# Kernel tuning notes

Hardware: AMD Instinct MI355X
Metric: run time of the kernel (lower is better)

Reference implementation:

```python
import jax, jax.numpy as jnp
import numpy as np

H = 64  # hidden size
T, B, I = 512, 4096, 2


def gru_layer(x_seq, Wih, Whh, bih, bhh):
    """PyTorch-semantics GRU layer. x_seq: [T,B,in]. Returns (all_h [T,B,H], h_last [B,H])."""
    # Precompute input-side gates for all timesteps in one GEMM: [T,B,3H]
    xg = jnp.einsum('tbi,gi->tbg', x_seq, Wih) + bih
    h0 = jnp.zeros((x_seq.shape[1], H), dtype=x_seq.dtype)

    def step(h, xg_t):
        hg = h @ Whh.T + bhh  # [B,3H]
        r = jax.nn.sigmoid(xg_t[:, :H] + hg[:, :H])
        z = jax.nn.sigmoid(xg_t[:, H:2 * H] + hg[:, H:2 * H])
        n = jnp.tanh(xg_t[:, 2 * H:] + r * hg[:, 2 * H:])
        h_new = (1.0 - z) * n + z * h
        return h_new, h_new

    h_last, hs = jax.lax.scan(step, h0, xg)
    return hs, h_last


def setup_inputs() -> dict:
    key = jax.random.key(0)
    ks = jax.random.split(key, 12)
    s = 0.125  # ~1/sqrt(H), matches PyTorch uniform init scale
    inp = {
        'x': jax.random.normal(ks[0], (T, B, I), dtype=jnp.float32),
        'Wih0': jax.random.normal(ks[1], (3 * H, I), dtype=jnp.float32) * s,
        'Whh0': jax.random.normal(ks[2], (3 * H, H), dtype=jnp.float32) * s,
        'bih0': jax.random.normal(ks[3], (3 * H,), dtype=jnp.float32) * s,
        'bhh0': jax.random.normal(ks[4], (3 * H,), dtype=jnp.float32) * s,
        'Wih1': jax.random.normal(ks[5], (3 * H, H), dtype=jnp.float32) * s,
        'Whh1': jax.random.normal(ks[6], (3 * H, H), dtype=jnp.float32) * s,
        'bih1': jax.random.normal(ks[7], (3 * H,), dtype=jnp.float32) * s,
        'bhh1': jax.random.normal(ks[8], (3 * H,), dtype=jnp.float32) * s,
        'Wp': jax.random.normal(ks[9], (1, 2 * H), dtype=jnp.float32) * s,
        'bp': jax.random.normal(ks[10], (1,), dtype=jnp.float32) * s,
    }
    return inp


def reference(x, Wih0, Whh0, bih0, bhh0, Wih1, Whh1, bih1, bhh1, Wp, bp):
    hs0, h0f = gru_layer(x, Wih0, Whh0, bih0, bhh0)     # layer 0 over input
    _, h1f = gru_layer(hs0, Wih1, Whh1, bih1, bhh1)      # layer 1 over layer-0 outputs
    feat = jnp.concatenate([h0f, h1f], axis=-1)          # h_n.permute(1,0,2).flatten(1) -> [B, 2H]
    out = feat @ Wp.T + bp                               # [B,1]
    return out.reshape(-1)
```

## Files before the change

### kernel.cpp

```cpp
#include <hip/hip_runtime.h>
#include <stdint.h>

#define TSTEPS 512
#define BATCH  4096
#define SROW 76

typedef __attribute__((ext_vector_type(8))) short bf16x8;
typedef __attribute__((ext_vector_type(4))) float f32x4;
typedef __attribute__((ext_vector_type(2))) float f32x2;

#define SRZ (-1.4426950408889634f)
#define SN  ( 2.8853900817779268f)

struct PX { f32x2 gr0, gz0, gn0, gr1, gz1, gn1; };

__device__ __forceinline__ short f2bf(float f) {
    uint32_t u = __float_as_uint(f);
    uint32_t r = (u + 0x7fffu + ((u >> 16) & 1u)) >> 16;
    return (short)r;
}
__device__ __forceinline__ uint32_t cvt_pk_bf16(float a, float b) {
    uint32_t r;
    asm("v_cvt_pk_bf16_f32 %0, %1, %2" : "=v"(r) : "v"(a), "v"(b));
    return r;
}
__device__ __forceinline__ float fast_rcp(float x) { return __builtin_amdgcn_rcpf(x); }
#if __has_builtin(__builtin_amdgcn_exp2f)
__device__ __forceinline__ float exp2_fast(float x) { return __builtin_amdgcn_exp2f(x); }
#else
__device__ __forceinline__ float exp2_fast(float x) { return __expf(x * 0.6931471805599453f); }
#endif

__device__ __forceinline__ f32x2 fma2(f32x2 a, f32x2 b, f32x2 c) {
    return __builtin_elementwise_fma(a, b, c);
}
__device__ __forceinline__ f32x2 splat2(float s) { return (f32x2){s, s}; }
__device__ __forceinline__ f32x2 exp22(f32x2 y) {
    return (f32x2){exp2_fast(y[0]), exp2_fast(y[1])};
}
__device__ __forceinline__ f32x2 rcp2(f32x2 y) {
    return (f32x2){fast_rcp(y[0]), fast_rcp(y[1])};
}
__device__ __forceinline__ f32x2 sig2(f32x2 y) {
    return rcp2(exp22(y) + splat2(1.0f));
}
__device__ __forceinline__ f32x2 gru_h(f32x2 yz, f32x2 yn, f32x2 h) {
    const f32x2 A = exp22(yz);
    const f32x2 B = exp22(yn);
    const f32x2 P = A * B;
    const f32x2 u = (P - A) + fma2(h, B, h);
    const f32x2 d = (P + A) + (B + splat2(1.0f));
    return u * rcp2(d);
}
__device__ __forceinline__ void bar_lgkm() {
    asm volatile("s_waitcnt lgkmcnt(0)\n\ts_barrier" ::: "memory");
}

__global__ __launch_bounds__(512, 2) void gru_fused(
    const float* __restrict__ x,
    const float* __restrict__ Wih0,
    const float* __restrict__ Whh0,
    const float* __restrict__ bih0,
    const float* __restrict__ bhh0,
    const float* __restrict__ Wih1,
    const float* __restrict__ Whh1,
    const float* __restrict__ bih1,
    const float* __restrict__ bhh1,
    const float* __restrict__ Wp,
    const float* __restrict__ bp,
    float* __restrict__ out)
{
    const int tid  = threadIdx.x;
    const int wv   = tid >> 6;
    const int isL0 = (wv < 4);
    const int w4   = wv & 3;
    const int l    = tid & 63;
    const int lm   = l & 15;
    const int lq   = l >> 4;
    const int b0   = blockIdx.x * 16;
    const int j    = w4 * 16 + lm;

    __shared__ short h0A[2][16 * SROW];
    __shared__ short h1A[2][16 * SROW];
    __shared__ float Pf[16][64];

    for (int idx = tid; idx < 2 * 16 * SROW; idx += 512) {
        ((short*)h0A)[idx] = 0;
        ((short*)h1A)[idx] = 0;
    }
    __syncthreads();

    const int aoff = lm * SROW + lq * 8;
    const int r0   = lq * 4;

    if (isL0) {
        bf16x8 w0[3][2];
#pragma unroll
        for (int g = 0; g < 3; ++g) {
            const int row = g * 64 + j;
            const float sc = (g == 2) ? SN : SRZ;
#pragma unroll
            for (int q = 0; q < 2; ++q) {
                const float* p = Whh0 + row * 64 + q * 32 + lq * 8;
                bf16x8 vh;
#pragma unroll
                for (int i = 0; i < 8; ++i) vh[i] = f2bf(p[i] * sc);
                w0[g][q] = vh;
            }
        }
        const f32x2 wr0 = splat2(SRZ * Wih0[j * 2 + 0]), wr1 = splat2(SRZ * Wih0[j * 2 + 1]);
        const f32x2 wz0 = splat2(SRZ * Wih0[(64 + j) * 2 + 0]), wz1 = splat2(SRZ * Wih0[(64 + j) * 2 + 1]);
        const f32x2 wn0 = splat2(SN * Wih0[(128 + j) * 2 + 0]), wn1 = splat2(SN * Wih0[(128 + j) * 2 + 1]);
        const float cb[3] = { SRZ * (bih0[j] + bhh0[j]),
                              SRZ * (bih0[64 + j] + bhh0[64 + j]),
                              SN  * bhh0[128 + j] };
        const f32x2 bn = splat2(SN * bih0[128 + j]);

        f32x2 h01 = {0.f, 0.f}, h23 = {0.f, 0.f};

        const float* xb_ = x + (size_t)(b0 + r0) * 2;
        f32x4 xEa = *(const f32x4*)xb_;
        f32x4 xEb = *(const f32x4*)(xb_ + 4);
        f32x4 xOa = *(const f32x4*)(xb_ + (size_t)BATCH * 2);
        f32x4 xOb = *(const f32x4*)(xb_ + (size_t)BATCH * 2 + 4);
        const float* xp = xb_ + 2 * (size_t)BATCH * 2;

        PX pE, pO;
        {
            const f32x2 x0a = {xEa[0], xEa[2]}, x1a = {xEa[1], xEa[3]};
            const f32x2 x0b = {xEb[0], xEb[2]}, x1b = {xEb[1], xEb[3]};
            pE.gr0 = fma2(wr0, x0a, wr1 * x1a);
            pE.gz0 = fma2(wz0, x0a, wz1 * x1a);
            pE.gn0 = fma2(wn0, x0a, fma2(wn1, x1a, bn));
            pE.gr1 = fma2(wr0, x0b, wr1 * x1b);
            pE.gz1 = fma2(wz0, x0b, wz1 * x1b);
            pE.gn1 = fma2(wn0, x0b, fma2(wn1, x1b, bn));
        }

        auto l0_step = [&](int pr, bool doload, PX& u, PX& d,
                           f32x4& xla, f32x4& xlb,
                           const f32x4& xsa, const f32x4& xsb) {
            const int pw = pr ^ 1;
            const bf16x8 a00 = *(const bf16x8*)&h0A[pr][aoff];
            const bf16x8 a01 = *(const bf16x8*)&h0A[pr][aoff + 32];
            if (doload) {
                xla = *(const f32x4*)xp;
                xlb = *(const f32x4*)(xp + 4);
                xp += (size_t)BATCH * 2;
            }
            f32x4 hg0[3];
            __builtin_amdgcn_s_setprio(1);
#pragma unroll
            for (int g = 0; g < 3; ++g) {
                const f32x4 ci = {cb[g], cb[g], cb[g], cb[g]};
                f32x4 c;
                c = __builtin_amdgcn_mfma_f32_16x16x32_bf16(a00, w0[g][0], ci, 0, 0, 0);
                hg0[g] = __builtin_amdgcn_mfma_f32_16x16x32_bf16(a01, w0[g][1], c, 0, 0, 0);
            }
            __builtin_amdgcn_s_setprio(0);
            {
                const f32x2 x0a = {xsa[0], xsa[2]}, x1a = {xsa[1], xsa[3]};
                const f32x2 x0b = {xsb[0], xsb[2]}, x1b = {xsb[1], xsb[3]};
                d.gr0 = fma2(wr0, x0a, wr1 * x1a);
                d.gz0 = fma2(wz0, x0a, wz1 * x1a);
                d.gn0 = fma2(wn0, x0a, fma2(wn1, x1a, bn));
                d.gr1 = fma2(wr0, x0b, wr1 * x1b);
                d.gz1 = fma2(wz0, x0b, wz1 * x1b);
                d.gn1 = fma2(wn0, x0b, fma2(wn1, x1b, bn));
            }
            {
                const f32x2 hgr = {hg0[0][0], hg0[0][1]};
                const f32x2 hgz = {hg0[1][0], hg0[1][1]};
                const f32x2 hgn = {hg0[2][0], hg0[2][1]};
                const f32x2 rv = sig2(hgr + u.gr0);
                const f32x2 hv = gru_h(hgz + u.gz0, fma2(rv, hgn, u.gn0), h01);
                h01 = hv;
                const uint32_t pk = cvt_pk_bf16(hv[0], hv[1]);
                h0A[pw][(r0 + 0) * SROW + j] = (short)(pk & 0xffffu);
                h0A[pw][(r0 + 1) * SROW + j] = (short)(pk >> 16);
            }
            {
                const f32x2 hgr = {hg0[0][2], hg0[0][3]};
                const f32x2 hgz = {hg0[1][2], hg0[1][3]};
                const f32x2 hgn = {hg0[2][2], hg0[2][3]};
                const f32x2 rv = sig2(hgr + u.gr1);
                const f32x2 hv = gru_h(hgz + u.gz1, fma2(rv, hgn, u.gn1), h23);
                h23 = hv;
                const uint32_t pk = cvt_pk_bf16(hv[0], hv[1]);
                h0A[pw][(r0 + 2) * SROW + j] = (short)(pk & 0xffffu);
                h0A[pw][(r0 + 3) * SROW + j] = (short)(pk >> 16);
            }
        };

        for (int tp = 0; tp < TSTEPS / 2; ++tp) {
            const bool doload = (tp < TSTEPS / 2 - 1);
            l0_step(0, doload, pE, pO, xEa, xEb, xOa, xOb);
            bar_lgkm();
            l0_step(1, doload, pO, pE, xOa, xOb, xEa, xEb);
            bar_lgkm();
        }

        const float wp0 = Wp[j];
        Pf[r0 + 0][j] = wp0 * h01[0];
        Pf[r0 + 1][j] = wp0 * h01[1];
        Pf[r0 + 2][j] = wp0 * h23[0];
        Pf[r0 + 3][j] = wp0 * h23[1];
        __syncthreads();
        __syncthreads();
    } else {
        bf16x8 w1[3][2], w2[3][2];
#pragma unroll
        for (int g = 0; g < 3; ++g) {
            const int row = g * 64 + j;
            const float sc = (g == 2) ? SN : SRZ;
#pragma unroll
            for (int q = 0; q < 2; ++q) {
                const float* p1 = Wih1 + row * 64 + q * 32 + lq * 8;
                const float* p2 = Whh1 + row * 64 + q * 32 + lq * 8;
                bf16x8 v1, v2;
#pragma unroll
                for (int i = 0; i < 8; ++i) {
                    v1[i] = f2bf(p1[i] * sc);
                    v2[i] = f2bf(p2[i] * sc);
                }
                w1[g][q] = v1; w2[g][q] = v2;
            }
        }
        const float cb[3] = { SRZ * (bih1[j] + bhh1[j]),
                              SRZ * (bih1[64 + j] + bhh1[64 + j]),
                              SN  * bih1[128 + j] };
        const float ce2 = SN * bhh1[128 + j];

        f32x2 h01 = {0.f, 0.f}, h23 = {0.f, 0.f};

        auto l1_step = [&](int pr, bool doew, bool dowrite) {
            const int pw = pr ^ 1;
            const bf16x8 a10 = *(const bf16x8*)&h1A[pr][aoff];
            const bf16x8 a11 = *(const bf16x8*)&h1A[pr][aoff + 32];
            const bf16x8 a00 = *(const bf16x8*)&h0A[pr][aoff];
            const bf16x8 a01 = *(const bf16x8*)&h0A[pr][aoff + 32];

            f32x4 xg1[3], hg1[3];
            __builtin_amdgcn_s_setprio(1);
#pragma unroll
            for (int g = 0; g < 3; ++g) {
                const float ev = (g == 2) ? ce2 : 0.0f;
                const f32x4 ei = {ev, ev, ev, ev};
                f32x4 e;
                e = __builtin_amdgcn_mfma_f32_16x16x32_bf16(a10, w2[g][0], ei, 0, 0, 0);
                hg1[g] = __builtin_amdgcn_mfma_f32_16x16x32_bf16(a11, w2[g][1], e, 0, 0, 0);
            }
#pragma unroll
            for (int g = 0; g < 3; ++g) {
                const f32x4 ci = {cb[g], cb[g], cb[g], cb[g]};
                f32x4 d;
                d = __builtin_amdgcn_mfma_f32_16x16x32_bf16(a00, w1[g][0], ci, 0, 0, 0);
                xg1[g] = __builtin_amdgcn_mfma_f32_16x16x32_bf16(a01, w1[g][1], d, 0, 0, 0);
            }
            __builtin_amdgcn_s_setprio(0);

            if (doew) {
                {
                    const f32x2 xgr = {xg1[0][0], xg1[0][1]}, hgr = {hg1[0][0], hg1[0][1]};
                    const f32x2 xgz = {xg1[1][0], xg1[1][1]}, hgz = {hg1[1][0], hg1[1][1]};
                    const f32x2 xgn = {xg1[2][0], xg1[2][1]}, hgn = {hg1[2][0], hg1[2][1]};
                    const f32x2 rv = sig2(xgr + hgr);
                    const f32x2 hv = gru_h(xgz + hgz, fma2(rv, hgn, xgn), h01);
                    h01 = hv;
                    if (dowrite) {
                        const uint32_t pk = cvt_pk_bf16(hv[0], hv[1]);
                        h1A[pw][(r0 + 0) * SROW + j] = (short)(pk & 0xffffu);
                        h1A[pw][(r0 + 1) * SROW + j] = (short)(pk >> 16);
                    }
                }
                {
                    const f32x2 xgr = {xg1[0][2], xg1[0][3]}, hgr = {hg1[0][2], hg1[0][3]};
                    const f32x2 xgz = {xg1[1][2], xg1[1][3]}, hgz = {hg1[1][2], hg1[1][3]};
                    const f32x2 xgn = {xg1[2][2], xg1[2][3]}, hgn = {hg1[2][2], hg1[2][3]};
                    const f32x2 rv = sig2(xgr + hgr);
                    const f32x2 hv = gru_h(xgz + hgz, fma2(rv, hgn, xgn), h23);
                    h23 = hv;
                    if (dowrite) {
                        const uint32_t pk = cvt_pk_bf16(hv[0], hv[1]);
                        h1A[pw][(r0 + 2) * SROW + j] = (short)(pk & 0xffffu);
                        h1A[pw][(r0 + 3) * SROW + j] = (short)(pk >> 16);
                    }
                }
            }
        };

        for (int tp = 0; tp < TSTEPS / 2; ++tp) {
            l1_step(0, tp > 0, true);
            bar_lgkm();
            l1_step(1, true, true);
            bar_lgkm();
        }
        l1_step(0, true, false);

        __syncthreads();
        const float wp1 = Wp[64 + j];
        Pf[r0 + 0][j] += wp1 * h01[0];
        Pf[r0 + 1][j] += wp1 * h01[1];
        Pf[r0 + 2][j] += wp1 * h23[0];
        Pf[r0 + 3][j] += wp1 * h23[1];
        __syncthreads();
    }

    if (tid < 16) {
        float s = bp[0];
#pragma unroll 8
        for (int k = 0; k < 64; ++k) s += Pf[tid][k];
        out[b0 + tid] = s;
    }
}

extern "C" void kernel_launch(void* const* d_in, const int* in_sizes, int n_in,
                              void* d_out, int out_size, void* d_ws, size_t ws_size,
                              hipStream_t stream) {
    (void)in_sizes; (void)n_in; (void)out_size; (void)d_ws; (void)ws_size;
    gru_fused<<<dim3(BATCH / 16), dim3(512), 0, stream>>>(
        (const float*)d_in[0], (const float*)d_in[1], (const float*)d_in[2],
        (const float*)d_in[3], (const float*)d_in[4], (const float*)d_in[5],
        (const float*)d_in[6], (const float*)d_in[7], (const float*)d_in[8],
        (const float*)d_in[9], (const float*)d_in[10], (float*)d_out);
}
```

Before: 329.2 us.

## Shrink blocks to 8 batch rows with 2 waves per layer and permlane compaction

Each block now handles 8 batch rows with 256 threads: two waves per layer, each covering 32 hidden units through two 16-column MFMA tiles. MFMA tiles stay 16 rows, so half of every MFMA output is padding. v_permlane32_swap compacts the valid rows so each lane's elementwise gate math covers 2 values instead of 4. Intended effect is twice as many blocks (512) with shorter per-step elementwise and store work, at the cost of wasted MFMA throughput and extra permlane ops.

```diff
diff --git a/kernel.cpp b/kernel.cpp
--- a/kernel.cpp
+++ b/kernel.cpp
@@ -8,11 +8,12 @@
 typedef __attribute__((ext_vector_type(8))) short bf16x8;
 typedef __attribute__((ext_vector_type(4))) float f32x4;
 typedef __attribute__((ext_vector_type(2))) float f32x2;
+typedef __attribute__((ext_vector_type(2))) unsigned int u32x2;
 
 #define SRZ (-1.4426950408889634f)
 #define SN  ( 2.8853900817779268f)
 
-struct PX { f32x2 gr0, gz0, gn0, gr1, gz1, gn1; };
+struct PX { f32x2 r[2], z[2], n[2]; };
 
 __device__ __forceinline__ short f2bf(float f) {
     uint32_t u = __float_as_uint(f);
@@ -55,8 +56,21 @@
 __device__ __forceinline__ void bar_lgkm() {
     asm volatile("s_waitcnt lgkmcnt(0)\n\ts_barrier" ::: "memory");
 }
-
-__global__ __launch_bounds__(512, 2) void gru_fused(
+__device__ __forceinline__ f32x2 compact2(f32x4 a) {
+#if __has_builtin(__builtin_amdgcn_permlane32_swap)
+    u32x2 r0 = __builtin_amdgcn_permlane32_swap(__float_as_uint(a[0]), __float_as_uint(a[2]), false, false);
+    u32x2 r1 = __builtin_amdgcn_permlane32_swap(__float_as_uint(a[1]), __float_as_uint(a[3]), false, false);
+    return (f32x2){__uint_as_float(r0[0]), __uint_as_float(r1[0])};
+#else
+    float u = a[0], s0 = a[2];
+    asm volatile("v_permlane32_swap_b32 %0, %1" : "+v"(u), "+v"(s0));
+    float v = a[1], s1 = a[3];
+    asm volatile("v_permlane32_swap_b32 %0, %1" : "+v"(v), "+v"(s1));
+    return (f32x2){u, v};
+#endif
+}
+
+__global__ __launch_bounds__(256, 2) void gru_fused(
     const float* __restrict__ x,
     const float* __restrict__ Wih0,
     const float* __restrict__ Whh0,
@@ -72,218 +86,208 @@
 {
     const int tid  = threadIdx.x;
     const int wv   = tid >> 6;
-    const int isL0 = (wv < 4);
-    const int w4   = wv & 3;
+    const int isL0 = (wv < 2);
+    const int wj   = wv & 1;
     const int l    = tid & 63;
     const int lm   = l & 15;
     const int lq   = l >> 4;
-    const int b0   = blockIdx.x * 16;
-    const int j    = w4 * 16 + lm;
+    const int rp   = (lq & 1) * 4 + (lq >> 1) * 2;
+    const int b0   = blockIdx.x * 8;
+    const int jb   = wj * 32 + lm;
 
     __shared__ short h0A[2][16 * SROW];
     __shared__ short h1A[2][16 * SROW];
-    __shared__ float Pf[16][64];
-
-    for (int idx = tid; idx < 2 * 16 * SROW; idx += 512) {
+    __shared__ float Pf[8][64];
+
+    for (int idx = tid; idx < 2 * 16 * SROW; idx += 256) {
         ((short*)h0A)[idx] = 0;
         ((short*)h1A)[idx] = 0;
     }
     __syncthreads();
 
     const int aoff = lm * SROW + lq * 8;
-    const int r0   = lq * 4;
 
     if (isL0) {
-        bf16x8 w0[3][2];
+        bf16x8 w0[3][2][2];
 #pragma unroll
         for (int g = 0; g < 3; ++g) {
-            const int row = g * 64 + j;
             const float sc = (g == 2) ? SN : SRZ;
 #pragma unroll
-            for (int q = 0; q < 2; ++q) {
-                const float* p = Whh0 + row * 64 + q * 32 + lq * 8;
-                bf16x8 vh;
-#pragma unroll
-                for (int i = 0; i < 8; ++i) vh[i] = f2bf(p[i] * sc);
-                w0[g][q] = vh;
-            }
-        }
-        const f32x2 wr0 = splat2(SRZ * Wih0[j * 2 + 0]), wr1 = splat2(SRZ * Wih0[j * 2 + 1]);
-        const f32x2 wz0 = splat2(SRZ * Wih0[(64 + j) * 2 + 0]), wz1 = splat2(SRZ * Wih0[(64 + j) * 2 + 1]);
-        const f32x2 wn0 = splat2(SN * Wih0[(128 + j) * 2 + 0]), wn1 = splat2(SN * Wih0[(128 + j) * 2 + 1]);
-        const float cb[3] = { SRZ * (bih0[j] + bhh0[j]),
-                              SRZ * (bih0[64 + j] + bhh0[64 + j]),
-                              SN  * bhh0[128 + j] };
-        const f32x2 bn = splat2(SN * bih0[128 + j]);
-
-        f32x2 h01 = {0.f, 0.f}, h23 = {0.f, 0.f};
-
-        const float* xb_ = x + (size_t)(b0 + r0) * 2;
-        f32x4 xEa = *(const f32x4*)xb_;
-        f32x4 xEb = *(const f32x4*)(xb_ + 4);
-        f32x4 xOa = *(const f32x4*)(xb_ + (size_t)BATCH * 2);
-        f32x4 xOb = *(const f32x4*)(xb_ + (size_t)BATCH * 2 + 4);
-        const float* xp = xb_ + 2 * (size_t)BATCH * 2;
+            for (int ti = 0; ti < 2; ++ti) {
+                const int row = g * 64 + jb + ti * 16;
+#pragma unroll
+                for (int q = 0; q < 2; ++q) {
+                    const float* p = Whh0 + row * 64 + q * 32 + lq * 8;
+                    bf16x8 vh;
+#pragma unroll
+                    for (int i = 0; i < 8; ++i) vh[i] = f2bf(p[i] * sc);
+                    w0[g][ti][q] = vh;
+                }
+            }
+        }
+        float wr0s[2], wr1s[2], wz0s[2], wz1s[2], wn0s[2], wn1s[2], bns[2];
+        float cb0[3][2];
+#pragma unroll
+        for (int ti = 0; ti < 2; ++ti) {
+            const int jj = jb + ti * 16;
+            wr0s[ti] = SRZ * Wih0[jj * 2 + 0];          wr1s[ti] = SRZ * Wih0[jj * 2 + 1];
+            wz0s[ti] = SRZ * Wih0[(64 + jj) * 2 + 0];   wz1s[ti] = SRZ * Wih0[(64 + jj) * 2 + 1];
+            wn0s[ti] = SN  * Wih0[(128 + jj) * 2 + 0];  wn1s[ti] = SN  * Wih0[(128 + jj) * 2 + 1];
+            bns[ti]  = SN  * bih0[128 + jj];
+            cb0[0][ti] = SRZ * (bih0[jj] + bhh0[jj]);
+            cb0[1][ti] = SRZ * (bih0[64 + jj] + bhh0[64 + jj]);
+            cb0[2][ti] = SN  * bhh0[128 + jj];
+        }
+
+        f32x2 hstv[2] = {{0.f, 0.f}, {0.f, 0.f}};
+
+        const float* xp = x + (size_t)(b0 + rp) * 2;
+        f32x4 xE = *(const f32x4*)xp;
+        f32x4 xO = *(const f32x4*)(xp + (size_t)BATCH * 2);
+        xp += 2 * (size_t)BATCH * 2;
 
         PX pE, pO;
         {
-            const f32x2 x0a = {xEa[0], xEa[2]}, x1a = {xEa[1], xEa[3]};
-            const f32x2 x0b = {xEb[0], xEb[2]}, x1b = {xEb[1], xEb[3]};
-            pE.gr0 = fma2(wr0, x0a, wr1 * x1a);
-            pE.gz0 = fma2(wz0, x0a, wz1 * x1a);
-            pE.gn0 = fma2(wn0, x0a, fma2(wn1, x1a, bn));
-            pE.gr1 = fma2(wr0, x0b, wr1 * x1b);
-            pE.gz1 = fma2(wz0, x0b, wz1 * x1b);
-            pE.gn1 = fma2(wn0, x0b, fma2(wn1, x1b, bn));
-        }
-
-        auto l0_step = [&](int pr, bool doload, PX& u, PX& d,
-                           f32x4& xla, f32x4& xlb,
-                           const f32x4& xsa, const f32x4& xsb) {
+            const f32x2 x0v = {xE[0], xE[2]}, x1v = {xE[1], xE[3]};
+#pragma unroll
+            for (int ti = 0; ti < 2; ++ti) {
+                pE.r[ti] = fma2(splat2(wr0s[ti]), x0v, splat2(wr1s[ti]) * x1v);
+                pE.z[ti] = fma2(splat2(wz0s[ti]), x0v, splat2(wz1s[ti]) * x1v);
+                pE.n[ti] = fma2(splat2(wn0s[ti]), x0v, fma2(splat2(wn1s[ti]), x1v, splat2(bns[ti])));
+            }
+        }
+
+        auto l0_step = [&](int pr, bool doload, PX& u, PX& d, f32x4& xl, const f32x4& xs) {
+            const int pw = pr ^ 1;
+            const bf16x8 a0 = *(const bf16x8*)&h0A[pr][aoff];
+            const bf16x8 a1 = *(const bf16x8*)&h0A[pr][aoff + 32];
+            if (doload) { xl = *(const f32x4*)xp; xp += (size_t)BATCH * 2; }
+            f32x4 hg[3][2];
+            __builtin_amdgcn_s_setprio(1);
+#pragma unroll
+            for (int ti = 0; ti < 2; ++ti)
+#pragma unroll
+                for (int g = 0; g < 3; ++g) {
+                    const f32x4 ci = {cb0[g][ti], cb0[g][ti], cb0[g][ti], cb0[g][ti]};
+                    f32x4 c;
+                    c = __builtin_amdgcn_mfma_f32_16x16x32_bf16(a0, w0[g][ti][0], ci, 0, 0, 0);
+                    hg[g][ti] = __builtin_amdgcn_mfma_f32_16x16x32_bf16(a1, w0[g][ti][1], c, 0, 0, 0);
+                }
+            __builtin_amdgcn_s_setprio(0);
+            {
+                const f32x2 x0v = {xs[0], xs[2]}, x1v = {xs[1], xs[3]};
+#pragma unroll
+                for (int ti = 0; ti < 2; ++ti) {
+                    d.r[ti] = fma2(splat2(wr0s[ti]), x0v, splat2(wr1s[ti]) * x1v);
+                    d.z[ti] = fma2(splat2(wz0s[ti]), x0v, splat2(wz1s[ti]) * x1v);
+                    d.n[ti] = fma2(splat2(wn0s[ti]), x0v, fma2(splat2(wn1s[ti]), x1v, splat2(bns[ti])));
+                }
+            }
+#pragma unroll
+            for (int ti = 0; ti < 2; ++ti) {
+                const f32x2 hgr = compact2(hg[0][ti]);
+                const f32x2 hgz = compact2(hg[1][ti]);
+                const f32x2 hgn = compact2(hg[2][ti]);
+                const f32x2 rv = sig2(hgr + u.r[ti]);
+                const f32x2 hv = gru_h(hgz + u.z[ti], fma2(rv, hgn, u.n[ti]), hstv[ti]);
+                hstv[ti] = hv;
+                const uint32_t pk = cvt_pk_bf16(hv[0], hv[1]);
+                const int jj = jb + ti * 16;
+                h0A[pw][(rp + 0) * SROW + jj] = (short)(pk & 0xffffu);
+                h0A[pw][(rp + 1) * SROW + jj] = (short)(pk >> 16);
+            }
+        };
+
+        for (int tp = 0; tp < TSTEPS / 2; ++tp) {
+            const bool dl = (tp < TSTEPS / 2 - 1);
+            l0_step(0, dl, pE, pO, xE, xO);
+            bar_lgkm();
+            l0_step(1, dl, pO, pE, xO, xE);
+            bar_lgkm();
+        }
+
+#pragma unroll
+        for (int ti = 0; ti < 2; ++ti) {
+            const int jj = jb + ti * 16;
+            const float wp0 = Wp[jj];
+            Pf[rp + 0][jj] = wp0 * hstv[ti][0];
+            Pf[rp + 1][jj] = wp0 * hstv[ti][1];
+        }
+        __syncthreads();
+        __syncthreads();
+    } else {
+        bf16x8 w1v[3][2][2], w2v[3][2][2];
+#pragma unroll
+        for (int g = 0; g < 3; ++g) {
+            const float sc = (g == 2) ? SN : SRZ;
+#pragma unroll
+            for (int ti = 0; ti < 2; ++ti) {
+                const int row = g * 64 + jb + ti * 16;
+#pragma unroll
+                for (int q = 0; q < 2; ++q) {
+                    const float* p1 = Wih1 + row * 64 + q * 32 + lq * 8;
+                    const float* p2 = Whh1 + row * 64 + q * 32 + lq * 8;
+                    bf16x8 v1, v2;
+#pragma unroll
+                    for (int i = 0; i < 8; ++i) {
+                        v1[i] = f2bf(p1[i] * sc);
+                        v2[i] = f2bf(p2[i] * sc);
+                    }
+                    w1v[g][ti][q] = v1; w2v[g][ti][q] = v2;
+                }
+            }
+        }
+        float cb1[3][2], ce2s[2];
+#pragma unroll
+        for (int ti = 0; ti < 2; ++ti) {
+            const int jj = jb + ti * 16;
+            cb1[0][ti] = SRZ * (bih1[jj] + bhh1[jj]);
+            cb1[1][ti] = SRZ * (bih1[64 + jj] + bhh1[64 + jj]);
+            cb1[2][ti] = SN  * bih1[128 + jj];
+            ce2s[ti]   = SN  * bhh1[128 + jj];
+        }
+
+        f32x2 hstv[2] = {{0.f, 0.f}, {0.f, 0.f}};
+
+        auto l1_step = [&](int pr, bool doew, bool dowrite) {
             const int pw = pr ^ 1;
             const bf16x8 a00 = *(const bf16x8*)&h0A[pr][aoff];
             const bf16x8 a01 = *(const bf16x8*)&h0A[pr][aoff + 32];
-            if (doload) {
-                xla = *(const f32x4*)xp;
-                xlb = *(const f32x4*)(xp + 4);
-                xp += (size_t)BATCH * 2;
-            }
-            f32x4 hg0[3];
-            __builtin_amdgcn_s_setprio(1);
-#pragma unroll
-            for (int g = 0; g < 3; ++g) {
-                const f32x4 ci = {cb[g], cb[g], cb[g], cb[g]};
-                f32x4 c;
-                c = __builtin_amdgcn_mfma_f32_16x16x32_bf16(a00, w0[g][0], ci, 0, 0, 0);
-                hg0[g] = __builtin_amdgcn_mfma_f32_16x16x32_bf16(a01, w0[g][1], c, 0, 0, 0);
-            }
-            __builtin_amdgcn_s_setprio(0);
-            {
-                const f32x2 x0a = {xsa[0], xsa[2]}, x1a = {xsa[1], xsa[3]};
-                const f32x2 x0b = {xsb[0], xsb[2]}, x1b = {xsb[1], xsb[3]};
-                d.gr0 = fma2(wr0, x0a, wr1 * x1a);
-                d.gz0 = fma2(wz0, x0a, wz1 * x1a);
-                d.gn0 = fma2(wn0, x0a, fma2(wn1, x1a, bn));
-                d.gr1 = fma2(wr0, x0b, wr1 * x1b);
-                d.gz1 = fma2(wz0, x0b, wz1 * x1b);
-                d.gn1 = fma2(wn0, x0b, fma2(wn1, x1b, bn));
-            }
-            {
-                const f32x2 hgr = {hg0[0][0], hg0[0][1]};
-                const f32x2 hgz = {hg0[1][0], hg0[1][1]};
-                const f32x2 hgn = {hg0[2][0], hg0[2][1]};
-                const f32x2 rv = sig2(hgr + u.gr0);
-                const f32x2 hv = gru_h(hgz + u.gz0, fma2(rv, hgn, u.gn0), h01);
-                h01 = hv;
-                const uint32_t pk = cvt_pk_bf16(hv[0], hv[1]);
-                h0A[pw][(r0 + 0) * SROW + j] = (short)(pk & 0xffffu);
-                h0A[pw][(r0 + 1) * SROW + j] = (short)(pk >> 16);
-            }
-            {
-                const f32x2 hgr = {hg0[0][2], hg0[0][3]};
-                const f32x2 hgz = {hg0[1][2], hg0[1][3]};
-                const f32x2 hgn = {hg0[2][2], hg0[2][3]};
-                const f32x2 rv = sig2(hgr + u.gr1);
-                const f32x2 hv = gru_h(hgz + u.gz1, fma2(rv, hgn, u.gn1), h23);
-                h23 = hv;
-                const uint32_t pk = cvt_pk_bf16(hv[0], hv[1]);
-                h0A[pw][(r0 + 2) * SROW + j] = (short)(pk & 0xffffu);
-                h0A[pw][(r0 + 3) * SROW + j] = (short)(pk >> 16);
-            }
-        };
-
-        for (int tp = 0; tp < TSTEPS / 2; ++tp) {
-            const bool doload = (tp < TSTEPS / 2 - 1);
-            l0_step(0, doload, pE, pO, xEa, xEb, xOa, xOb);
-            bar_lgkm();
-            l0_step(1, doload, pO, pE, xOa, xOb, xEa, xEb);
-            bar_lgkm();
-        }
-
-        const float wp0 = Wp[j];
-        Pf[r0 + 0][j] = wp0 * h01[0];
-        Pf[r0 + 1][j] = wp0 * h01[1];
-        Pf[r0 + 2][j] = wp0 * h23[0];
-        Pf[r0 + 3][j] = wp0 * h23[1];
-        __syncthreads();
-        __syncthreads();
-    } else {
-        bf16x8 w1[3][2], w2[3][2];
-#pragma unroll
-        for (int g = 0; g < 3; ++g) {
-            const int row = g * 64 + j;
-            const float sc = (g == 2) ? SN : SRZ;
-#pragma unroll
-            for (int q = 0; q < 2; ++q) {
-                const float* p1 = Wih1 + row * 64 + q * 32 + lq * 8;
-                const float* p2 = Whh1 + row * 64 + q * 32 + lq * 8;
-                bf16x8 v1, v2;
-#pragma unroll
-                for (int i = 0; i < 8; ++i) {
-                    v1[i] = f2bf(p1[i] * sc);
-                    v2[i] = f2bf(p2[i] * sc);
-                }
-                w1[g][q] = v1; w2[g][q] = v2;
-            }
-        }
-        const float cb[3] = { SRZ * (bih1[j] + bhh1[j]),
-                              SRZ * (bih1[64 + j] + bhh1[64 + j]),
-                              SN  * bih1[128 + j] };
-        const float ce2 = SN * bhh1[128 + j];
-
-        f32x2 h01 = {0.f, 0.f}, h23 = {0.f, 0.f};
-
-        auto l1_step = [&](int pr, bool doew, bool dowrite) {
-            const int pw = pr ^ 1;
             const bf16x8 a10 = *(const bf16x8*)&h1A[pr][aoff];
             const bf16x8 a11 = *(const bf16x8*)&h1A[pr][aoff + 32];
-            const bf16x8 a00 = *(const bf16x8*)&h0A[pr][aoff];
-            const bf16x8 a01 = *(const bf16x8*)&h0A[pr][aoff + 32];
-
-            f32x4 xg1[3], hg1[3];
+            f32x4 xg[3][2], hgv[3][2];
             __builtin_amdgcn_s_setprio(1);
 #pragma unroll
-            for (int g = 0; g < 3; ++g) {
-                const float ev = (g == 2) ? ce2 : 0.0f;
-                const f32x4 ei = {ev, ev, ev, ev};
-                f32x4 e;
-                e = __builtin_amdgcn_mfma_f32_16x16x32_bf16(a10, w2[g][0], ei, 0, 0, 0);
-                hg1[g] = __builtin_amdgcn_mfma_f32_16x16x32_bf16(a11, w2[g][1], e, 0, 0, 0);
-            }
-#pragma unroll
-            for (int g = 0; g < 3; ++g) {
-                const f32x4 ci = {cb[g], cb[g], cb[g], cb[g]};
-                f32x4 d;
-                d = __builtin_amdgcn_mfma_f32_16x16x32_bf16(a00, w1[g][0], ci, 0, 0, 0);
-                xg1[g] = __builtin_amdgcn_mfma_f32_16x16x32_bf16(a01, w1[g][1], d, 0, 0, 0);
-            }
+            for (int ti = 0; ti < 2; ++ti)
+#pragma unroll
+                for (int g = 0; g < 3; ++g) {
+                    const f32x4 ci = {cb1[g][ti], cb1[g][ti], cb1[g][ti], cb1[g][ti]};
+                    f32x4 dd;
+                    dd = __builtin_amdgcn_mfma_f32_16x16x32_bf16(a00, w1v[g][ti][0], ci, 0, 0, 0);
+                    xg[g][ti] = __builtin_amdgcn_mfma_f32_16x16x32_bf16(a01, w1v[g][ti][1], dd, 0, 0, 0);
+                    const float ev = (g == 2) ? ce2s[ti] : 0.0f;
+                    const f32x4 ei = {ev, ev, ev, ev};
+                    f32x4 e;
+                    e = __builtin_amdgcn_mfma_f32_16x16x32_bf16(a10, w2v[g][ti][0], ei, 0, 0, 0);
+                    hgv[g][ti] = __builtin_amdgcn_mfma_f32_16x16x32_bf16(a11, w2v[g][ti][1], e, 0, 0, 0);
+                }
             __builtin_amdgcn_s_setprio(0);
 
             if (doew) {
-                {
-                    const f32x2 xgr = {xg1[0][0], xg1[0][1]}, hgr = {hg1[0][0], hg1[0][1]};
-                    const f32x2 xgz = {xg1[1][0], xg1[1][1]}, hgz = {hg1[1][0], hg1[1][1]};
-                    const f32x2 xgn = {xg1[2][0], xg1[2][1]}, hgn = {hg1[2][0], hg1[2][1]};
-                    const f32x2 rv = sig2(xgr + hgr);
-                    const f32x2 hv = gru_h(xgz + hgz, fma2(rv, hgn, xgn), h01);
-                    h01 = hv;
+#pragma unroll
+                for (int ti = 0; ti < 2; ++ti) {
+                    const f32x2 r2  = compact2(xg[0][ti] + hgv[0][ti]);
+                    const f32x2 z2  = compact2(xg[1][ti] + hgv[1][ti]);
+                    const f32x2 xn2 = compact2(xg[2][ti]);
+                    const f32x2 hn2 = compact2(hgv[2][ti]);
+                    const f32x2 rv = sig2(r2);
+                    const f32x2 hv = gru_h(z2, fma2(rv, hn2, xn2), hstv[ti]);
+                    hstv[ti] = hv;
                     if (dowrite) {
                         const uint32_t pk = cvt_pk_bf16(hv[0], hv[1]);
-                        h1A[pw][(r0 + 0) * SROW + j] = (short)(pk & 0xffffu);
-                        h1A[pw][(r0 + 1) * SROW + j] = (short)(pk >> 16);
-                    }
-                }
-                {
-                    const f32x2 xgr = {xg1[0][2], xg1[0][3]}, hgr = {hg1[0][2], hg1[0][3]};
-                    const f32x2 xgz = {xg1[1][2], xg1[1][3]}, hgz = {hg1[1][2], hg1[1][3]};
-                    const f32x2 xgn = {xg1[2][2], xg1[2][3]}, hgn = {hg1[2][2], hg1[2][3]};
-                    const f32x2 rv = sig2(xgr + hgr);
-                    const f32x2 hv = gru_h(xgz + hgz, fma2(rv, hgn, xgn), h23);
-                    h23 = hv;
-                    if (dowrite) {
-                        const uint32_t pk = cvt_pk_bf16(hv[0], hv[1]);
-                        h1A[pw][(r0 + 2) * SROW + j] = (short)(pk & 0xffffu);
-                        h1A[pw][(r0 + 3) * SROW + j] = (short)(pk >> 16);
+                        const int jj = jb + ti * 16;
+                        h1A[pw][(rp + 0) * SROW + jj] = (short)(pk & 0xffffu);
+                        h1A[pw][(rp + 1) * SROW + jj] = (short)(pk >> 16);
                     }
                 }
             }
@@ -298,15 +302,17 @@
         l1_step(0, true, false);
 
         __syncthreads();
-        const float wp1 = Wp[64 + j];
-        Pf[r0 + 0][j] += wp1 * h01[0];
-        Pf[r0 + 1][j] += wp1 * h01[1];
-        Pf[r0 + 2][j] += wp1 * h23[0];
-        Pf[r0 + 3][j] += wp1 * h23[1];
+#pragma unroll
+        for (int ti = 0; ti < 2; ++ti) {
+            const int jj = jb + ti * 16;
+            const float wp1 = Wp[64 + jj];
+            Pf[rp + 0][jj] += wp1 * hstv[ti][0];
+            Pf[rp + 1][jj] += wp1 * hstv[ti][1];
+        }
         __syncthreads();
     }
 
-    if (tid < 16) {
+    if (tid < 8) {
         float s = bp[0];
 #pragma unroll 8
         for (int k = 0; k < 64; ++k) s += Pf[tid][k];
@@ -318,7 +324,7 @@
                               void* d_out, int out_size, void* d_ws, size_t ws_size,
                               hipStream_t stream) {
     (void)in_sizes; (void)n_in; (void)out_size; (void)d_ws; (void)ws_size;
-    gru_fused<<<dim3(BATCH / 16), dim3(512), 0, stream>>>(
+    gru_fused<<<dim3(BATCH / 8), dim3(256), 0, stream>>>(
         (const float*)d_in[0], (const float*)d_in[1], (const float*)d_in[2],
         (const float*)d_in[3], (const float*)d_in[4], (const float*)d_in[5],
         (const float*)d_in[6], (const float*)d_in[7], (const float*)d_in[8],
```

New measurement: 482.3 us. +46.5%, slower.
